# Performance work log

Hardware: AMD Instinct MI355X
Metric: run time of the kernel (lower is better)

## Reference

```python
import jax, jax.numpy as jnp
import numpy as np

NUM_ROUTES = 2048
IN_CH = 32
NUM_CAPS = 32
OUT_CH = 32
NUM_ITER = 3
BATCH = 64


def setup_inputs() -> dict:
    key = jax.random.key(0)
    kx, kw = jax.random.split(key)
    x = jax.random.normal(kx, (BATCH, NUM_ROUTES, IN_CH), dtype=jnp.float32)
    # W matches nn.Parameter torch.randn(1, routes, caps, out, in); drop leading 1
    W = jax.random.normal(kw, (NUM_ROUTES, NUM_CAPS, OUT_CH, IN_CH), dtype=jnp.float32)
    return {"x": x, "W": W}


def _squash(s):
    # Faithful to original: norm taken over the trailing singleton dim,
    # i.e. elementwise: sq = s^2, out = sq*s / ((1+sq)*sqrt(sq))
    sq = s * s
    return sq * s / ((1.0 + sq) * jnp.sqrt(sq))


def reference(x, W):
    # u_hat[b,r,c,o] = W[r,c,o,:] @ x[b,r,:]
    u_hat = jnp.einsum('rcoi,bri->brco', W, x)  # [B,R,C,O]
    R, C = W.shape[0], W.shape[1]
    b_ij = jnp.zeros((R, C), dtype=x.dtype)
    v = None
    for it in range(NUM_ITER):
        c_ij = jax.nn.softmax(b_ij, axis=0)              # softmax over routes (dim=1 in torch)
        s = jnp.einsum('rc,brco->bco', c_ij, u_hat)      # [B,C,O]
        v = _squash(s)
        if it < NUM_ITER - 1:
            # agreement: <u_hat, v> over O, then batch-mean update of logits
            a = jnp.einsum('brco,bco->brc', u_hat, v)    # [B,R,C]
            b_ij = b_ij + a.mean(axis=0)
    return v[..., None]  # [B, num_capsules, out_channels, 1], matches v_j.squeeze(1)
```

## Files before the change

kernel.cpp:

```cpp
#include <hip/hip_runtime.h>


#define B_  64
#define R_  2048
#define CI  32
#define NC  32
#define OC  32
#define NCO 1024
#define RPB 16
#define GR  (R_ / RPB)
#define NG  8
#define NSL 128
#define BN  65536

typedef __attribute__((ext_vector_type(8))) short bf16x8;
typedef __attribute__((ext_vector_type(4))) float f32x4;

static constexpr long WN = (long)R_ * NCO * CI;
static constexpr long XN = (long)B_ * R_ * CI;

__device__ __forceinline__ unsigned short rne_bf16(float f) {
  unsigned int u = __builtin_bit_cast(unsigned int, f);
  u += 0x7fffu + ((u >> 16) & 1u);
  return (unsigned short)(u >> 16);
}

__device__ __forceinline__ bf16x8 pack8(f32x4 a, f32x4 b) {
  bf16x8 r;
  r[0] = (short)rne_bf16(a[0]); r[1] = (short)rne_bf16(a[1]);
  r[2] = (short)rne_bf16(a[2]); r[3] = (short)rne_bf16(a[3]);
  r[4] = (short)rne_bf16(b[0]); r[5] = (short)rne_bf16(b[1]);
  r[6] = (short)rne_bf16(b[2]); r[7] = (short)rne_bf16(b[3]);
  return r;
}

__global__ __launch_bounds__(256) void cvt_kernel(const float* __restrict__ src,
                                                  unsigned short* __restrict__ dst,
                                                  int n4) {
  int i = blockIdx.x * blockDim.x + threadIdx.x;
  int stride = gridDim.x * blockDim.x;
  const f32x4* s4 = (const f32x4*)src;
  ushort4* d4 = (ushort4*)dst;
  for (; i < n4; i += stride) {
    f32x4 f = s4[i];
    ushort4 u;
    u.x = rne_bf16(f[0]); u.y = rne_bf16(f[1]);
    u.z = rne_bf16(f[2]); u.w = rne_bf16(f[3]);
    d4[i] = u;
  }
}

__global__ __launch_bounds__(256) void cvtW_kernel(const float* __restrict__ src,
                                                   unsigned short* __restrict__ dst) {
  long i = (long)blockIdx.x * 256 + threadIdx.x;
  const long stride = (long)gridDim.x * 256;
  const long n8 = WN / 8;
  const f32x4* s4 = (const f32x4*)src;
  bf16x8* d8 = (bf16x8*)dst;
  for (; i < n8; i += stride) {
    f32x4 a = __builtin_nontemporal_load(s4 + 2 * i);
    f32x4 b = __builtin_nontemporal_load(s4 + 2 * i + 1);
    d8[i] = pack8(a, b);
  }
}

template<bool FAST, bool UNIFORM>
__global__ __launch_bounds__(256, 4) void s_kernel(
    const float* __restrict__ x, const float* __restrict__ W,
    const unsigned short* __restrict__ xb, const unsigned short* __restrict__ Wb,
    const float* __restrict__ cmat,
    float* __restrict__ part) {
  const int tid  = threadIdx.x;
  const int lane = tid & 63;
  const int mw   = tid >> 6;
  const int g    = blockIdx.y;
  const int r0   = blockIdx.x * RPB;
  const int l15  = lane & 15;
  const int q    = lane >> 4;
  const int k0   = q * 8;
  const int bA   = mw * 16 + l15;

  f32x4 acc[8];
#pragma unroll
  for (int t = 0; t < 8; ++t) acc[t] = (f32x4){0.f, 0.f, 0.f, 0.f};
  const f32x4 zero4 = (f32x4){0.f, 0.f, 0.f, 0.f};

  for (int j = 0; j < RPB; ++j) {
    const int r = r0 + j;
    bf16x8 af;
    if (FAST) {
      af = *(const bf16x8*)(xb + ((bA * R_ + r) * CI + k0));
    } else {
      const f32x4* xp = (const f32x4*)(x + ((bA * R_ + r) * CI + k0));
      af = pack8(xp[0], xp[1]);
    }
    bf16x8 wf[8];
#pragma unroll
    for (int t = 0; t < 8; ++t) {
      const int nrow = g * NSL + t * 16 + l15;
      const int wof = (r * NCO + nrow) * CI + k0;
      if (FAST) wf[t] = *(const bf16x8*)(Wb + wof);
      else {
        const f32x4* wp = (const f32x4*)(W + wof);
        wf[t] = pack8(wp[0], wp[1]);
      }
    }
    if (UNIFORM) {
#pragma unroll
      for (int t = 0; t < 8; ++t)
        acc[t] = __builtin_amdgcn_mfma_f32_16x16x32_bf16(af, wf[t], acc[t], 0, 0, 0);
    } else {
      float cv[4];
#pragma unroll
      for (int cc = 0; cc < 4; ++cc) cv[cc] = cmat[(g * 4 + cc) * R_ + r];
#pragma unroll
      for (int t = 0; t < 8; ++t) {
        f32x4 u = __builtin_amdgcn_mfma_f32_16x16x32_bf16(af, wf[t], zero4, 0, 0, 0);
        acc[t] += cv[t >> 1] * u;
      }
    }
  }
  const int pbase = blockIdx.x * BN;
#pragma unroll
  for (int t = 0; t < 8; ++t) {
    const int n = g * NSL + t * 16 + l15;
#pragma unroll
    for (int rr = 0; rr < 4; ++rr) {
      const int b = mw * 16 + q * 4 + rr;
      part[pbase + b * NCO + n] = UNIFORM ? acc[t][rr] * (1.0f / 2048.0f)
                                          : acc[t][rr];
    }
  }
}

__global__ __launch_bounds__(256) void rs1_kernel(const float* __restrict__ part,
                                                  float* __restrict__ part2) {
  const int i4 = blockIdx.x * 256 + threadIdx.x;
  const int ip = blockIdx.y;
  const f32x4* p4 = (const f32x4*)part;
  f32x4 s = (f32x4){0.f, 0.f, 0.f, 0.f};
#pragma unroll
  for (int p = 0; p < 16; ++p) s += p4[(ip * 16 + p) * (BN / 4) + i4];
  ((f32x4*)part2)[ip * (BN / 4) + i4] = s;
}

__global__ __launch_bounds__(256) void rs2_kernel(const float* __restrict__ part2,
                                                  float* __restrict__ o) {
  const int i4 = blockIdx.x * 256 + threadIdx.x;
  const f32x4* p4 = (const f32x4*)part2;
  f32x4 s = (f32x4){0.f, 0.f, 0.f, 0.f};
#pragma unroll
  for (int ip = 0; ip < 8; ++ip) s += p4[ip * (BN / 4) + i4];
  f32x4 r;
#pragma unroll
  for (int c = 0; c < 4; ++c) {
    const float sv = s[c];
    const float sq = sv * sv;
    r[c] = sq * sv / ((1.0f + sq) * sqrtf(sq));
  }
  ((f32x4*)o)[i4] = r;
}

template<bool FAST, bool FIRST>
__global__ __launch_bounds__(256, 4) void a_kernel(
    const float* __restrict__ x, const float* __restrict__ W,
    const unsigned short* __restrict__ xb, const unsigned short* __restrict__ Wb,
    const float* __restrict__ v,
    float* __restrict__ bb) {
  const int tid  = threadIdx.x;
  const int lane = tid & 63;
  const int mw   = tid >> 6;
  const int g    = blockIdx.y;
  const int r0   = blockIdx.x * RPB;
  const int l15  = lane & 15;
  const int q    = lane >> 4;
  const int k0   = q * 8;
  const int bA   = mw * 16 + l15;

  __shared__ float slab[4][32][65];
  __shared__ float accw[2][4][64];

  float vreg[8][4];
#pragma unroll
  for (int t = 0; t < 8; ++t) {
    const int n = g * NSL + t * 16 + l15;
#pragma unroll
    for (int rr = 0; rr < 4; ++rr)
      vreg[t][rr] = v[(mw * 16 + q * 4 + rr) * NCO + n];
  }
  const f32x4 zero4 = (f32x4){0.f, 0.f, 0.f, 0.f};

  for (int kk = 0; kk < 2; ++kk) {
    for (int jj = 0; jj < 8; ++jj) {
      const int r = r0 + kk * 8 + jj;
      bf16x8 af;
      if (FAST) {
        af = *(const bf16x8*)(xb + ((bA * R_ + r) * CI + k0));
      } else {
        const f32x4* xp = (const f32x4*)(x + ((bA * R_ + r) * CI + k0));
        af = pack8(xp[0], xp[1]);
      }
      bf16x8 wf[8];
#pragma unroll
      for (int t = 0; t < 8; ++t) {
        const int nrow = g * NSL + t * 16 + l15;
        const int wof = (r * NCO + nrow) * CI + k0;
        if (FAST) wf[t] = *(const bf16x8*)(Wb + wof);
        else {
          const f32x4* wp = (const f32x4*)(W + wof);
          wf[t] = pack8(wp[0], wp[1]);
        }
      }
      float dotc[4] = {0.f, 0.f, 0.f, 0.f};
#pragma unroll
      for (int t = 0; t < 8; ++t) {
        f32x4 u = __builtin_amdgcn_mfma_f32_16x16x32_bf16(af, wf[t], zero4, 0, 0, 0);
        dotc[t >> 1] += u[0] * vreg[t][0] + u[1] * vreg[t][1] +
                        u[2] * vreg[t][2] + u[3] * vreg[t][3];
      }
#pragma unroll
      for (int cc = 0; cc < 4; ++cc)
        slab[mw][cc * 8 + jj][lane] = dotc[cc];
    }
    {
      const int p = lane >> 1, h = lane & 1;
      float sm = 0.f;
#pragma unroll
      for (int i = 0; i < 32; ++i) sm += slab[mw][p][h * 32 + i];
      accw[kk][mw][lane] = sm;
    }
  }
  __syncthreads();
  if (tid < 64) {
    const int kk = tid >> 5;
    const int p  = tid & 31;
    float tot = 0.f;
#pragma unroll
    for (int w = 0; w < 4; ++w)
      tot += accw[kk][w][p * 2] + accw[kk][w][p * 2 + 1];
    const int cc = p >> 3, jj = p & 7;
    const int r  = r0 + kk * 8 + jj;
    const int o  = (g * 4 + cc) * R_ + r;
    const float val = tot * (1.0f / 64.0f);
    bb[o] = FIRST ? val : (bb[o] + val);
  }
}

__global__ __launch_bounds__(256) void softmax_kernel(const float* __restrict__ bb,
                                                      float* __restrict__ cmat) {
  const int c = blockIdx.x;
  const int tid = threadIdx.x;
  __shared__ float red[8];
  float m = -1e30f;
  for (int r = tid; r < R_; r += 256) m = fmaxf(m, bb[c * R_ + r]);
#pragma unroll
  for (int s = 1; s < 64; s <<= 1) m = fmaxf(m, __shfl_xor(m, s));
  if ((tid & 63) == 0) red[tid >> 6] = m;
  __syncthreads();
  m = fmaxf(fmaxf(red[0], red[1]), fmaxf(red[2], red[3]));
  float sum = 0.f;
  for (int r = tid; r < R_; r += 256) sum += __expf(bb[c * R_ + r] - m);
#pragma unroll
  for (int s = 1; s < 64; s <<= 1) sum += __shfl_xor(sum, s);
  if ((tid & 63) == 0) red[4 + (tid >> 6)] = sum;
  __syncthreads();
  sum = red[4] + red[5] + red[6] + red[7];
  const float inv = 1.0f / sum;
  for (int r = tid; r < R_; r += 256)
    cmat[c * R_ + r] = __expf(bb[c * R_ + r] - m) * inv;
}

extern "C" void kernel_launch(void* const* d_in, const int* in_sizes, int n_in,
                              void* d_out, int out_size, void* d_ws, size_t ws_size,
                              hipStream_t stream) {
  const float* x = (const float*)d_in[0];
  const float* W = (const float*)d_in[1];
  float* out = (float*)d_out;

  char* ws = (char*)d_ws;
  float* bb    = (float*)(ws);
  float* cmat  = (float*)(ws + (1 << 18));
  float* vbuf  = (float*)(ws + 2 * (size_t)(1 << 18));
  float* part2 = (float*)(ws + (1 << 20));
  float* part  = (float*)(ws + 4 * (size_t)(1 << 20));
  unsigned short* Wb = (unsigned short*)(ws + 36 * (size_t)(1 << 20));
  unsigned short* xb = (unsigned short*)(ws + 36 * (size_t)(1 << 20) + WN * 2);
  const size_t need_fast = 36 * (size_t)(1 << 20) + (size_t)WN * 2 + (size_t)XN * 2;
  const bool fast = ws_size >= need_fast;

  const dim3 grid(GR, NG);
  const dim3 rgrid(BN / 1024, 8);

  if (fast) {
    cvt_kernel<<<1024, 256, 0, stream>>>(x, xb, (int)(XN / 4));
    cvtW_kernel<<<2048, 256, 0, stream>>>(W, Wb);
    s_kernel<true, true><<<grid, 256, 0, stream>>>(x, W, xb, Wb, nullptr, part);
  } else {
    s_kernel<false, true><<<grid, 256, 0, stream>>>(x, W, xb, Wb, nullptr, part);
  }
  rs1_kernel<<<rgrid, 256, 0, stream>>>(part, part2);
  rs2_kernel<<<BN / 1024, 256, 0, stream>>>(part2, vbuf);

  if (fast) a_kernel<true, true><<<grid, 256, 0, stream>>>(x, W, xb, Wb, vbuf, bb);
  else      a_kernel<false, true><<<grid, 256, 0, stream>>>(x, W, xb, Wb, vbuf, bb);
  softmax_kernel<<<NC, 256, 0, stream>>>(bb, cmat);
  if (fast) s_kernel<true, false><<<grid, 256, 0, stream>>>(x, W, xb, Wb, cmat, part);
  else      s_kernel<false, false><<<grid, 256, 0, stream>>>(x, W, xb, Wb, cmat, part);
  rs1_kernel<<<rgrid, 256, 0, stream>>>(part, part2);
  rs2_kernel<<<BN / 1024, 256, 0, stream>>>(part2, vbuf);

  if (fast) a_kernel<true, false><<<grid, 256, 0, stream>>>(x, W, xb, Wb, vbuf, bb);
  else      a_kernel<false, false><<<grid, 256, 0, stream>>>(x, W, xb, Wb, vbuf, bb);
  softmax_kernel<<<NC, 256, 0, stream>>>(bb, cmat);
  if (fast) s_kernel<true, false><<<grid, 256, 0, stream>>>(x, W, xb, Wb, cmat, part);
  else      s_kernel<false, false><<<grid, 256, 0, stream>>>(x, W, xb, Wb, cmat, part);
  rs1_kernel<<<rgrid, 256, 0, stream>>>(part, part2);
  rs2_kernel<<<BN / 1024, 256, 0, stream>>>(part2, out);
}
```

Measured before the change: 612.7 us.

## Software-pipeline operand loads in s/a kernels, unroll conversion and softmax

Adds register double-buffering to s_kernel and a_kernel, so the x/W fragments (and routing coefficients) for the next route are loaded while the MFMAs for the current route run. The launch-bounds occupancy hint drops from 4 to 3 waves to leave room for the extra registers. cvtW_kernel now issues four nontemporal load pairs per thread per iteration, and the partial-sum stores and reads use nontemporal hints. softmax keeps its 8 values per thread in registers instead of reading bb three times. Lower occupancy and higher register pressure could offset the gain from hiding load latency.

```diff
diff --git a/kernel.cpp b/kernel.cpp
--- a/kernel.cpp
+++ b/kernel.cpp
@@ -42,7 +42,7 @@
   const f32x4* s4 = (const f32x4*)src;
   ushort4* d4 = (ushort4*)dst;
   for (; i < n4; i += stride) {
-    f32x4 f = s4[i];
+    f32x4 f = __builtin_nontemporal_load(s4 + i);
     ushort4 u;
     u.x = rne_bf16(f[0]); u.y = rne_bf16(f[1]);
     u.z = rne_bf16(f[2]); u.w = rne_bf16(f[3]);
@@ -52,20 +52,46 @@
 
 __global__ __launch_bounds__(256) void cvtW_kernel(const float* __restrict__ src,
                                                    unsigned short* __restrict__ dst) {
-  long i = (long)blockIdx.x * 256 + threadIdx.x;
-  const long stride = (long)gridDim.x * 256;
   const long n8 = WN / 8;
   const f32x4* s4 = (const f32x4*)src;
   bf16x8* d8 = (bf16x8*)dst;
-  for (; i < n8; i += stride) {
-    f32x4 a = __builtin_nontemporal_load(s4 + 2 * i);
-    f32x4 b = __builtin_nontemporal_load(s4 + 2 * i + 1);
-    d8[i] = pack8(a, b);
-  }
+  long base = (long)blockIdx.x * 1024 + threadIdx.x;
+  const long stride = (long)gridDim.x * 1024;
+  for (; base < n8; base += stride) {
+    f32x4 a[4], b[4];
+#pragma unroll
+    for (int u = 0; u < 4; ++u) {
+      const long gi = base + u * 256;
+      a[u] = __builtin_nontemporal_load(s4 + 2 * gi);
+      b[u] = __builtin_nontemporal_load(s4 + 2 * gi + 1);
+    }
+#pragma unroll
+    for (int u = 0; u < 4; ++u)
+      d8[base + u * 256] = pack8(a[u], b[u]);
+  }
+}
+
+template<bool FAST>
+__device__ __forceinline__ bf16x8 ld_af(const float* __restrict__ x,
+                                        const unsigned short* __restrict__ xb,
+                                        int bA, int r, int k0) {
+  if (FAST) return *(const bf16x8*)(xb + ((bA * R_ + r) * CI + k0));
+  const f32x4* xp = (const f32x4*)(x + ((bA * R_ + r) * CI + k0));
+  return pack8(xp[0], xp[1]);
+}
+
+template<bool FAST>
+__device__ __forceinline__ bf16x8 ld_wf(const float* __restrict__ W,
+                                        const unsigned short* __restrict__ Wb,
+                                        int r, int nrow, int k0) {
+  const int wof = (r * NCO + nrow) * CI + k0;
+  if (FAST) return *(const bf16x8*)(Wb + wof);
+  const f32x4* wp = (const f32x4*)(W + wof);
+  return pack8(wp[0], wp[1]);
 }
 
 template<bool FAST, bool UNIFORM>
-__global__ __launch_bounds__(256, 4) void s_kernel(
+__global__ __launch_bounds__(256, 3) void s_kernel(
     const float* __restrict__ x, const float* __restrict__ W,
     const unsigned short* __restrict__ xb, const unsigned short* __restrict__ Wb,
     const float* __restrict__ cmat,
@@ -85,38 +111,50 @@
   for (int t = 0; t < 8; ++t) acc[t] = (f32x4){0.f, 0.f, 0.f, 0.f};
   const f32x4 zero4 = (f32x4){0.f, 0.f, 0.f, 0.f};
 
+  bf16x8 afc = ld_af<FAST>(x, xb, bA, r0, k0);
+  bf16x8 wfc[8];
+#pragma unroll
+  for (int t = 0; t < 8; ++t)
+    wfc[t] = ld_wf<FAST>(W, Wb, r0, g * NSL + t * 16 + l15, k0);
+  float cvc[4];
+  if (!UNIFORM) {
+#pragma unroll
+    for (int cc = 0; cc < 4; ++cc) cvc[cc] = cmat[(g * 4 + cc) * R_ + r0];
+  }
+
+#pragma unroll
   for (int j = 0; j < RPB; ++j) {
-    const int r = r0 + j;
-    bf16x8 af;
-    if (FAST) {
-      af = *(const bf16x8*)(xb + ((bA * R_ + r) * CI + k0));
+    bf16x8 afn, wfn[8];
+    float cvn[4];
+    if (j + 1 < RPB) {
+      const int rn = r0 + j + 1;
+      afn = ld_af<FAST>(x, xb, bA, rn, k0);
+#pragma unroll
+      for (int t = 0; t < 8; ++t)
+        wfn[t] = ld_wf<FAST>(W, Wb, rn, g * NSL + t * 16 + l15, k0);
+      if (!UNIFORM) {
+#pragma unroll
+        for (int cc = 0; cc < 4; ++cc) cvn[cc] = cmat[(g * 4 + cc) * R_ + rn];
+      }
+    }
+    if (UNIFORM) {
+#pragma unroll
+      for (int t = 0; t < 8; ++t)
+        acc[t] = __builtin_amdgcn_mfma_f32_16x16x32_bf16(afc, wfc[t], acc[t], 0, 0, 0);
     } else {
-      const f32x4* xp = (const f32x4*)(x + ((bA * R_ + r) * CI + k0));
-      af = pack8(xp[0], xp[1]);
-    }
-    bf16x8 wf[8];
-#pragma unroll
-    for (int t = 0; t < 8; ++t) {
-      const int nrow = g * NSL + t * 16 + l15;
-      const int wof = (r * NCO + nrow) * CI + k0;
-      if (FAST) wf[t] = *(const bf16x8*)(Wb + wof);
-      else {
-        const f32x4* wp = (const f32x4*)(W + wof);
-        wf[t] = pack8(wp[0], wp[1]);
+#pragma unroll
+      for (int t = 0; t < 8; ++t) {
+        f32x4 u = __builtin_amdgcn_mfma_f32_16x16x32_bf16(afc, wfc[t], zero4, 0, 0, 0);
+        acc[t] += cvc[t >> 1] * u;
       }
     }
-    if (UNIFORM) {
-#pragma unroll
-      for (int t = 0; t < 8; ++t)
-        acc[t] = __builtin_amdgcn_mfma_f32_16x16x32_bf16(af, wf[t], acc[t], 0, 0, 0);
-    } else {
-      float cv[4];
-#pragma unroll
-      for (int cc = 0; cc < 4; ++cc) cv[cc] = cmat[(g * 4 + cc) * R_ + r];
-#pragma unroll
-      for (int t = 0; t < 8; ++t) {
-        f32x4 u = __builtin_amdgcn_mfma_f32_16x16x32_bf16(af, wf[t], zero4, 0, 0, 0);
-        acc[t] += cv[t >> 1] * u;
+    if (j + 1 < RPB) {
+      afc = afn;
+#pragma unroll
+      for (int t = 0; t < 8; ++t) wfc[t] = wfn[t];
+      if (!UNIFORM) {
+#pragma unroll
+        for (int cc = 0; cc < 4; ++cc) cvc[cc] = cvn[cc];
       }
     }
   }
@@ -127,8 +165,8 @@
 #pragma unroll
     for (int rr = 0; rr < 4; ++rr) {
       const int b = mw * 16 + q * 4 + rr;
-      part[pbase + b * NCO + n] = UNIFORM ? acc[t][rr] * (1.0f / 2048.0f)
-                                          : acc[t][rr];
+      const float val = UNIFORM ? acc[t][rr] * (1.0f / 2048.0f) : acc[t][rr];
+      __builtin_nontemporal_store(val, &part[pbase + b * NCO + n]);
     }
   }
 }
@@ -140,7 +178,8 @@
   const f32x4* p4 = (const f32x4*)part;
   f32x4 s = (f32x4){0.f, 0.f, 0.f, 0.f};
 #pragma unroll
-  for (int p = 0; p < 16; ++p) s += p4[(ip * 16 + p) * (BN / 4) + i4];
+  for (int p = 0; p < 16; ++p)
+    s += __builtin_nontemporal_load(p4 + (ip * 16 + p) * (BN / 4) + i4);
   ((f32x4*)part2)[ip * (BN / 4) + i4] = s;
 }
 
@@ -162,7 +201,7 @@
 }
 
 template<bool FAST, bool FIRST>
-__global__ __launch_bounds__(256, 4) void a_kernel(
+__global__ __launch_bounds__(256, 3) void a_kernel(
     const float* __restrict__ x, const float* __restrict__ W,
     const unsigned short* __restrict__ xb, const unsigned short* __restrict__ Wb,
     const float* __restrict__ v,
@@ -190,44 +229,44 @@
   }
   const f32x4 zero4 = (f32x4){0.f, 0.f, 0.f, 0.f};
 
-  for (int kk = 0; kk < 2; ++kk) {
-    for (int jj = 0; jj < 8; ++jj) {
-      const int r = r0 + kk * 8 + jj;
-      bf16x8 af;
-      if (FAST) {
-        af = *(const bf16x8*)(xb + ((bA * R_ + r) * CI + k0));
-      } else {
-        const f32x4* xp = (const f32x4*)(x + ((bA * R_ + r) * CI + k0));
-        af = pack8(xp[0], xp[1]);
-      }
-      bf16x8 wf[8];
-#pragma unroll
-      for (int t = 0; t < 8; ++t) {
-        const int nrow = g * NSL + t * 16 + l15;
-        const int wof = (r * NCO + nrow) * CI + k0;
-        if (FAST) wf[t] = *(const bf16x8*)(Wb + wof);
-        else {
-          const f32x4* wp = (const f32x4*)(W + wof);
-          wf[t] = pack8(wp[0], wp[1]);
-        }
-      }
-      float dotc[4] = {0.f, 0.f, 0.f, 0.f};
-#pragma unroll
-      for (int t = 0; t < 8; ++t) {
-        f32x4 u = __builtin_amdgcn_mfma_f32_16x16x32_bf16(af, wf[t], zero4, 0, 0, 0);
-        dotc[t >> 1] += u[0] * vreg[t][0] + u[1] * vreg[t][1] +
-                        u[2] * vreg[t][2] + u[3] * vreg[t][3];
-      }
-#pragma unroll
-      for (int cc = 0; cc < 4; ++cc)
-        slab[mw][cc * 8 + jj][lane] = dotc[cc];
-    }
-    {
+  bf16x8 afc = ld_af<FAST>(x, xb, bA, r0, k0);
+  bf16x8 wfc[8];
+#pragma unroll
+  for (int t = 0; t < 8; ++t)
+    wfc[t] = ld_wf<FAST>(W, Wb, r0, g * NSL + t * 16 + l15, k0);
+
+#pragma unroll
+  for (int j = 0; j < RPB; ++j) {
+    bf16x8 afn, wfn[8];
+    if (j + 1 < RPB) {
+      const int rn = r0 + j + 1;
+      afn = ld_af<FAST>(x, xb, bA, rn, k0);
+#pragma unroll
+      for (int t = 0; t < 8; ++t)
+        wfn[t] = ld_wf<FAST>(W, Wb, rn, g * NSL + t * 16 + l15, k0);
+    }
+    float dotc[4] = {0.f, 0.f, 0.f, 0.f};
+#pragma unroll
+    for (int t = 0; t < 8; ++t) {
+      f32x4 u = __builtin_amdgcn_mfma_f32_16x16x32_bf16(afc, wfc[t], zero4, 0, 0, 0);
+      dotc[t >> 1] += u[0] * vreg[t][0] + u[1] * vreg[t][1] +
+                      u[2] * vreg[t][2] + u[3] * vreg[t][3];
+    }
+#pragma unroll
+    for (int cc = 0; cc < 4; ++cc)
+      slab[mw][cc * 8 + (j & 7)][lane] = dotc[cc];
+    if ((j & 7) == 7) {
+      const int kk = j >> 3;
       const int p = lane >> 1, h = lane & 1;
       float sm = 0.f;
 #pragma unroll
       for (int i = 0; i < 32; ++i) sm += slab[mw][p][h * 32 + i];
       accw[kk][mw][lane] = sm;
+    }
+    if (j + 1 < RPB) {
+      afc = afn;
+#pragma unroll
+      for (int t = 0; t < 8; ++t) wfc[t] = wfn[t];
     }
   }
   __syncthreads();
@@ -251,23 +290,32 @@
   const int c = blockIdx.x;
   const int tid = threadIdx.x;
   __shared__ float red[8];
-  float m = -1e30f;
-  for (int r = tid; r < R_; r += 256) m = fmaxf(m, bb[c * R_ + r]);
+  float vals[8];
+#pragma unroll
+  for (int k = 0; k < 8; ++k) vals[k] = bb[c * R_ + k * 256 + tid];
+  float m = vals[0];
+#pragma unroll
+  for (int k = 1; k < 8; ++k) m = fmaxf(m, vals[k]);
 #pragma unroll
   for (int s = 1; s < 64; s <<= 1) m = fmaxf(m, __shfl_xor(m, s));
   if ((tid & 63) == 0) red[tid >> 6] = m;
   __syncthreads();
   m = fmaxf(fmaxf(red[0], red[1]), fmaxf(red[2], red[3]));
   float sum = 0.f;
-  for (int r = tid; r < R_; r += 256) sum += __expf(bb[c * R_ + r] - m);
+#pragma unroll
+  for (int k = 0; k < 8; ++k) {
+    vals[k] = __expf(vals[k] - m);
+    sum += vals[k];
+  }
 #pragma unroll
   for (int s = 1; s < 64; s <<= 1) sum += __shfl_xor(sum, s);
   if ((tid & 63) == 0) red[4 + (tid >> 6)] = sum;
   __syncthreads();
   sum = red[4] + red[5] + red[6] + red[7];
   const float inv = 1.0f / sum;
-  for (int r = tid; r < R_; r += 256)
-    cmat[c * R_ + r] = __expf(bb[c * R_ + r] - m) * inv;
+#pragma unroll
+  for (int k = 0; k < 8; ++k)
+    cmat[c * R_ + k * 256 + tid] = vals[k] * inv;
 }
 
 extern "C" void kernel_launch(void* const* d_in, const int* in_sizes, int n_in,
```

Result: slower. 1.004 ms (+63.8%).
